# Performance work log

Measured on AMD Instinct MI355X. Metric: run time of the kernel, lower is better.

The kernel has to match this reference:

```python
import jax, jax.numpy as jnp
import numpy as np

S = 256          # seq_len
H = 1024         # hidden_size == input_size (required by inputs + hf add)
NUM_ITER = 1     # interaction module inner iterations
EPS = 1e-5       # BatchNorm1d eps


def setup_inputs() -> dict:
    key = jax.random.key(0)
    ks = jax.random.split(key, 16)
    xav = np.sqrt(2.0 / (H + H))          # xavier_normal for HxH dense
    u = 1.0 / np.sqrt(H)                  # torch LSTMCell default init scale
    inp = {"inputs": jax.random.normal(ks[0], (S, H), jnp.float32)}
    # interaction module dense layers
    for i in range(4):
        inp[f"W{i+1}"] = jax.random.normal(ks[1 + i], (H, H), jnp.float32) * xav
        inp[f"b{i+1}"] = jnp.zeros((H,), jnp.float32)
    # LSTM cells (forward / backward)
    inp["Wih_f"] = jax.random.uniform(ks[5], (4 * H, H), jnp.float32, -u, u)
    inp["Whh_f"] = jax.random.uniform(ks[6], (4 * H, H), jnp.float32, -u, u)
    inp["bih_f"] = jax.random.uniform(ks[7], (4 * H,), jnp.float32, -u, u)
    inp["bhh_f"] = jax.random.uniform(ks[8], (4 * H,), jnp.float32, -u, u)
    inp["Wih_b"] = jax.random.uniform(ks[9], (4 * H, H), jnp.float32, -u, u)
    inp["Whh_b"] = jax.random.uniform(ks[10], (4 * H, H), jnp.float32, -u, u)
    inp["bih_b"] = jax.random.uniform(ks[11], (4 * H,), jnp.float32, -u, u)
    inp["bhh_b"] = jax.random.uniform(ks[12], (4 * H,), jnp.float32, -u, u)
    # BatchNorm1d affine params (default init)
    inp["gamma_f"] = jnp.ones((H,), jnp.float32)
    inp["beta_f"] = jnp.zeros((H,), jnp.float32)
    inp["gamma_b"] = jnp.ones((H,), jnp.float32)
    inp["beta_b"] = jnp.zeros((H,), jnp.float32)
    return inp


def _bn(x, g, b):
    # training-mode BatchNorm1d over the batch (seq) axis, biased variance
    m = jnp.mean(x, axis=0)
    xc = x - m
    v = jnp.mean(xc * xc, axis=0)
    return xc * jax.lax.rsqrt(v + EPS) * g + b


def _lstm_c(x, h, c, Wih, Whh, bih, bhh):
    # torch LSTMCell: returns new cell state only (as used by the module)
    g = x @ Wih.T + bih + h @ Whh.T + bhh
    i, f, gg, o = jnp.split(g, 4)
    return jax.nn.sigmoid(f) * c + jax.nn.sigmoid(i) * jnp.tanh(gg)


def reference(inputs, W1, b1, W2, b2, W3, b3, W4, b4,
              Wih_f, Whh_f, bih_f, bhh_f, Wih_b, Whh_b, bih_b, bhh_b,
              gamma_f, beta_f, gamma_b, beta_b):
    sig = jax.nn.sigmoid

    def interaction(x0, hf, hb):
        for _ in range(NUM_ITER):
            x1 = sig((x0 + hf) @ W1.T + b1)
            hb2 = sig((hb + x1) @ W2.T + b2)
            hf2 = sig((x1 + hf) @ W3.T + b3)
            x0 = sig((hb2 + x1) @ W4.T + b4)
            hf, hb = hf2, hb2
        return x0, hf, hb

    def step(carry, t):
        hf, hb, fc, bc = carry
        _, hf2, hb2 = interaction(inputs, hf, hb)
        out = (hf2 + hb2) * 0.5  # value returned at the last timestep (pre-BN)
        tb = S - 1 - t
        fc = fc.at[t].set(_lstm_c(inputs[t], hf2[t], fc[t], Wih_f, Whh_f, bih_f, bhh_f))
        bc = bc.at[tb].set(_lstm_c(inputs[tb], hb2[tb], bc[tb], Wih_b, Whh_b, bih_b, bhh_b))
        hf_n = _bn(hf2, gamma_f, beta_f)
        hb_n = _bn(hb2, gamma_b, beta_b)
        return (hf_n, hb_n, fc, bc), out

    z = jnp.zeros((S, H), jnp.float32)
    (_, _, _, _), outs = jax.lax.scan(step, (z, z, z, z), jnp.arange(S))
    return outs[-1]  # [S, H]
```

## Files before the change

### kernel.cpp

```cpp
#include <hip/hip_runtime.h>
#include <hip/hip_bf16.h>
#include <math.h>

#define S 256
#define H 1024
#define SH (S*H)
#define EPS 1e-5f

typedef float f32x4 __attribute__((ext_vector_type(4)));
typedef short bf16x8 __attribute__((ext_vector_type(8)));

__device__ __forceinline__ float sigm(float x){ return 1.0f/(1.0f+expf(-x)); }

__device__ __forceinline__ ushort f2bf(float a){
    union { __hip_bfloat16 b; ushort u; } cv;
    cv.b = __float2bfloat16(a);
    return cv.u;
}
__device__ __forceinline__ float bf2f(ushort u){
    union { __hip_bfloat16 b; ushort u; } cv; cv.u = u;
    return __bfloat162float(cv.b);
}

__device__ __forceinline__ int xcd_swizzle(unsigned gbx) {
    return (int)((gbx & 7u) * 32u + (gbx >> 3));
}

__global__ __launch_bounds__(256) void k_pack(const float* __restrict__ W,
                                              ushort* __restrict__ ph,
                                              ushort* __restrict__ pl) {
    int p  = blockIdx.x * 256 + threadIdx.x;
    int l  = p & 63;
    int kt = (p >> 6) & 31;
    int jt = p >> 11;
    int j  = jt * 16 + (l & 15);
    int k0 = kt * 32 + ((l >> 4) << 3);
    const float* src = W + j * H + k0;
    float4 a0 = *(const float4*)src;
    float4 a1 = *(const float4*)(src + 4);
    float av[8] = {a0.x,a0.y,a0.z,a0.w,a1.x,a1.y,a1.z,a1.w};
    bf16x8 vh, vl;
#pragma unroll
    for (int e = 0; e < 8; ++e) {
        ushort h = f2bf(av[e]);
        vh[e] = (short)h;
        vl[e] = (short)f2bf(av[e] - bf2f(h));
    }
    *(bf16x8*)(ph + (size_t)p * 8) = vh;
    *(bf16x8*)(pl + (size_t)p * 8) = vl;
}

__global__ __launch_bounds__(256) void k_init(float* __restrict__ stats,
                                              unsigned* __restrict__ sync) {
    int t = blockIdx.x * 256 + threadIdx.x;
    if (t < 8 * H) stats[t] = 0.0f;
    if (t == 0) { sync[0] = 0u; sync[64] = 0u; }
}

__device__ __forceinline__ void grid_barrier(unsigned* ctrp, unsigned* flagp,
                                             unsigned want) {
    __syncthreads();
    if (threadIdx.x == 0) {
        __threadfence();
        unsigned old = __hip_atomic_fetch_add(ctrp, 1u, __ATOMIC_RELAXED,
                                              __HIP_MEMORY_SCOPE_AGENT);
        if (old == want * 256u - 1u) {
            __hip_atomic_store(flagp, want, __ATOMIC_RELEASE,
                               __HIP_MEMORY_SCOPE_AGENT);
        } else {
            while (__hip_atomic_load(flagp, __ATOMIC_RELAXED,
                                     __HIP_MEMORY_SCOPE_AGENT) < want)
                __builtin_amdgcn_s_sleep(1);
        }
        __threadfence();
    }
    __syncthreads();
}

__global__ __launch_bounds__(256) void k_persist(
    const float* __restrict__ X,
    const ushort* __restrict__ wp1h, const ushort* __restrict__ wp1l,
    const ushort* __restrict__ wp2h, const ushort* __restrict__ wp2l,
    const ushort* __restrict__ wp3h, const ushort* __restrict__ wp3l,
    const float* __restrict__ b1v, const float* __restrict__ b2v,
    const float* __restrict__ b3v,
    const float* __restrict__ gFv, const float* __restrict__ bFv,
    const float* __restrict__ gBv, const float* __restrict__ bBv,
    ushort* __restrict__ A2h, ushort* __restrict__ A2l,
    ushort* __restrict__ A3h, ushort* __restrict__ A3l,
    float* __restrict__ rawf, float* __restrict__ rawb,
    float* __restrict__ stats, float* __restrict__ outp,
    unsigned* __restrict__ syncv)
{
    __shared__ __align__(16) ushort lhs_hi[8192];
    __shared__ __align__(16) ushort lhs_lo[8192];
    __shared__ float scF[H], ofF[H];
    __shared__ float red[4][64][2];

    const int t = threadIdx.x;
    const int g = xcd_swizzle(blockIdx.x);
    const int sb = g & 7, jb = g >> 3;
    const int lane = t & 63, w = t >> 6;
    const int wr = w >> 1, wc = w & 1;
    const int row0 = sb * 32;
    const int jt = jb * 2 + wc;
    const int j = jt * 16 + (lane & 15);
    const int arow = row0 + wr * 16 + (lane & 15);
    const int koff = (lane >> 4) << 3;
    const int srow = row0 + wr * 16 + ((lane >> 4) << 2);
    const float inv = 1.0f / (float)S;

    unsigned* ctrp  = syncv;
    unsigned* flagp = syncv + 64;
    unsigned bgen = 0;

    for (int s = 0; s < S; ++s) {
        const int p = (s + 1) & 1, q = s & 1;
        const int first = (s == 0);
        const float* stP = stats + q * 4 * H;
        float* stA = stats + p * 4 * H;
        const float* rF = rawf + q * SH;
        const float* rB = rawb + q * SH;
        float* wF = rawf + p * SH;
        float* wB = rawb + p * SH;

        if (!first) {
            for (int k = t; k < H; k += 256) {
                float m = stP[k] * inv;
                float v = stP[H + k] * inv - m * m;
                float sc = rsqrtf(v + EPS) * gFv[k];
                scF[k] = sc;
                ofF[k] = bFv[k] - m * sc;
            }
        }
        __syncthreads();

        {
            f32x4 acc0 = {0,0,0,0}, acc1 = {0,0,0,0}, acc2 = {0,0,0,0};
            for (int phase = 0; phase < 4; ++phase) {
                int kbase = phase << 8;
#pragma unroll
                for (int it = 0; it < 4; ++it) {
                    int gg = t + (it << 8);
                    int si = gg & 31, kg = gg >> 5;
                    int k = kbase + (kg << 3);
                    const float* xp = X + (row0 + si) * H + k;
                    float4 x0 = *(const float4*)xp;
                    float4 x1 = *(const float4*)(xp + 4);
                    float a[8] = {x0.x,x0.y,x0.z,x0.w,x1.x,x1.y,x1.z,x1.w};
                    if (!first) {
                        const float* rp = rF + (row0 + si) * H + k;
                        float4 r0 = *(const float4*)rp;
                        float4 r1 = *(const float4*)(rp + 4);
                        float rr[8] = {r0.x,r0.y,r0.z,r0.w,r1.x,r1.y,r1.z,r1.w};
#pragma unroll
                        for (int e = 0; e < 8; ++e)
                            a[e] += rr[e] * scF[k + e] + ofF[k + e];
                    }
                    bf16x8 vh, vl;
#pragma unroll
                    for (int e = 0; e < 8; ++e) {
                        ushort h = f2bf(a[e]);
                        vh[e] = (short)h;
                        vl[e] = (short)f2bf(a[e] - bf2f(h));
                    }
                    int idx = ((((si >> 4) * 8 + (kg >> 2)) * 64) +
                               (((kg & 3) << 4) | (si & 15))) * 8;
                    *(bf16x8*)(lhs_hi + idx) = vh;
                    *(bf16x8*)(lhs_lo + idx) = vl;
                }
                __syncthreads();
                const ushort* bph = wp1h + ((size_t)(jt * 32 + (phase << 3)) * 64 + lane) * 8;
                const ushort* bpl = wp1l + ((size_t)(jt * 32 + (phase << 3)) * 64 + lane) * 8;
                const ushort* ah  = lhs_hi + ((wr * 8) * 64 + lane) * 8;
                const ushort* al  = lhs_lo + ((wr * 8) * 64 + lane) * 8;
#pragma unroll
                for (int kc = 0; kc < 8; ++kc) {
                    bf16x8 a_h = *(const bf16x8*)(ah + kc * 512);
                    bf16x8 a_l = *(const bf16x8*)(al + kc * 512);
                    bf16x8 b_h = *(const bf16x8*)(bph + kc * 512);
                    bf16x8 b_l = *(const bf16x8*)(bpl + kc * 512);
                    acc0 = __builtin_amdgcn_mfma_f32_16x16x32_bf16(a_h, b_h, acc0, 0, 0, 0);
                    acc1 = __builtin_amdgcn_mfma_f32_16x16x32_bf16(a_h, b_l, acc1, 0, 0, 0);
                    acc2 = __builtin_amdgcn_mfma_f32_16x16x32_bf16(a_l, b_h, acc2, 0, 0, 0);
                }
                __syncthreads();
            }

            float bias = b1v[j];
            float scFj = 0.f, ofFj = 0.f, scBj = 0.f, ofBj = 0.f;
            if (!first) {
                scFj = scF[j]; ofFj = ofF[j];
                float m = stP[2 * H + j] * inv;
                float v = stP[3 * H + j] * inv - m * m;
                scBj = rsqrtf(v + EPS) * gBv[j];
                ofBj = bBv[j] - m * scBj;
            }
            f32x4 sum = acc0 + acc1 + acc2;
#pragma unroll
            for (int r = 0; r < 4; ++r) {
                int o = (srow + r) * H + j;
                float x1v = sigm(sum[r] + bias);
                float hb_ = first ? 0.f : rB[o] * scBj + ofBj;
                float hf_ = first ? 0.f : rF[o] * scFj + ofFj;
                float a2 = hb_ + x1v;
                float a3 = x1v + hf_;
                ushort h2 = f2bf(a2);
                A2h[o] = h2;
                A2l[o] = f2bf(a2 - bf2f(h2));
                ushort h3 = f2bf(a3);
                A3h[o] = h3;
                A3l[o] = f2bf(a3 - bf2f(h3));
            }
        }

        grid_barrier(ctrp, flagp, ++bgen);

        if (blockIdx.x == 0) {
            float* z = stats + q * 4 * H;
            for (int k = t; k < 4 * H; k += 256) z[k] = 0.0f;
        }

        float vb[4];
        {
            f32x4 acc0 = {0,0,0,0}, acc1 = {0,0,0,0}, acc2 = {0,0,0,0};
            const ushort* ah = A2h + arow * H + koff;
            const ushort* al = A2l + arow * H + koff;
            const ushort* bh = wp2h + ((size_t)(jt * 32) * 64 + lane) * 8;
            const ushort* bl = wp2l + ((size_t)(jt * 32) * 64 + lane) * 8;
#pragma unroll 8
            for (int kc = 0; kc < 32; ++kc) {
                bf16x8 vah = *(const bf16x8*)(ah + kc * 32);
                bf16x8 val = *(const bf16x8*)(al + kc * 32);
                bf16x8 vbh = *(const bf16x8*)(bh + kc * 512);
                bf16x8 vbl = *(const bf16x8*)(bl + kc * 512);
                acc0 = __builtin_amdgcn_mfma_f32_16x16x32_bf16(vah, vbh, acc0, 0, 0, 0);
                acc1 = __builtin_amdgcn_mfma_f32_16x16x32_bf16(vah, vbl, acc1, 0, 0, 0);
                acc2 = __builtin_amdgcn_mfma_f32_16x16x32_bf16(val, vbh, acc2, 0, 0, 0);
            }
            f32x4 sum = acc0 + acc1 + acc2;
            float bias = b2v[j];
            float ts = 0.f, tq = 0.f;
#pragma unroll
            for (int r = 0; r < 4; ++r) {
                float v = sigm(sum[r] + bias);
                vb[r] = v;
                wB[(srow + r) * H + j] = v;
                ts += v; tq += v * v;
            }
            red[w][lane][0] = ts;
            red[w][lane][1] = tq;
        }
        __syncthreads();
        if (t < 32) {
            int wc2 = t >> 4, jl = t & 15;
            int jj = jb * 32 + wc2 * 16 + jl;
            float ts = 0.f, tq = 0.f;
#pragma unroll
            for (int wr2 = 0; wr2 < 2; ++wr2)
#pragma unroll
                for (int lg = 0; lg < 4; ++lg) {
                    ts += red[wr2 * 2 + wc2][lg * 16 + jl][0];
                    tq += red[wr2 * 2 + wc2][lg * 16 + jl][1];
                }
            atomicAdd(&stA[2 * H + jj], ts);
            atomicAdd(&stA[3 * H + jj], tq);
        }
        __syncthreads();

        {
            f32x4 acc0 = {0,0,0,0}, acc1 = {0,0,0,0}, acc2 = {0,0,0,0};
            const ushort* ah = A3h + arow * H + koff;
            const ushort* al = A3l + arow * H + koff;
            const ushort* bh = wp3h + ((size_t)(jt * 32) * 64 + lane) * 8;
            const ushort* bl = wp3l + ((size_t)(jt * 32) * 64 + lane) * 8;
#pragma unroll 8
            for (int kc = 0; kc < 32; ++kc) {
                bf16x8 vah = *(const bf16x8*)(ah + kc * 32);
                bf16x8 val = *(const bf16x8*)(al + kc * 32);
                bf16x8 vbh = *(const bf16x8*)(bh + kc * 512);
                bf16x8 vbl = *(const bf16x8*)(bl + kc * 512);
                acc0 = __builtin_amdgcn_mfma_f32_16x16x32_bf16(vah, vbh, acc0, 0, 0, 0);
                acc1 = __builtin_amdgcn_mfma_f32_16x16x32_bf16(vah, vbl, acc1, 0, 0, 0);
                acc2 = __builtin_amdgcn_mfma_f32_16x16x32_bf16(val, vbh, acc2, 0, 0, 0);
            }
            f32x4 sum = acc0 + acc1 + acc2;
            float bias = b3v[j];
            float ts = 0.f, tq = 0.f;
#pragma unroll
            for (int r = 0; r < 4; ++r) {
                float v = sigm(sum[r] + bias);
                wF[(srow + r) * H + j] = v;
                if (s == S - 1)
                    outp[(srow + r) * H + j] = 0.5f * (v + vb[r]);
                ts += v; tq += v * v;
            }
            red[w][lane][0] = ts;
            red[w][lane][1] = tq;
        }
        __syncthreads();
        if (t < 32) {
            int wc2 = t >> 4, jl = t & 15;
            int jj = jb * 32 + wc2 * 16 + jl;
            float ts = 0.f, tq = 0.f;
#pragma unroll
            for (int wr2 = 0; wr2 < 2; ++wr2)
#pragma unroll
                for (int lg = 0; lg < 4; ++lg) {
                    ts += red[wr2 * 2 + wc2][lg * 16 + jl][0];
                    tq += red[wr2 * 2 + wc2][lg * 16 + jl][1];
                }
            atomicAdd(&stA[0 * H + jj], ts);
            atomicAdd(&stA[1 * H + jj], tq);
        }

        if (s != S - 1)
            grid_barrier(ctrp, flagp, ++bgen);
    }
}

extern "C" void kernel_launch(void* const* d_in, const int* in_sizes, int n_in,
                              void* d_out, int out_size, void* d_ws, size_t ws_size,
                              hipStream_t stream) {
    (void)in_sizes; (void)n_in; (void)out_size; (void)ws_size;

    const float* X  = (const float*)d_in[0];
    const float* W1 = (const float*)d_in[1];
    const float* b1 = (const float*)d_in[2];
    const float* W2 = (const float*)d_in[3];
    const float* b2 = (const float*)d_in[4];
    const float* W3 = (const float*)d_in[5];
    const float* b3 = (const float*)d_in[6];
    const float* gf = (const float*)d_in[17];
    const float* bf = (const float*)d_in[18];
    const float* gb = (const float*)d_in[19];
    const float* bb = (const float*)d_in[20];

    char* base = (char*)d_ws;
    const size_t MB = 1024 * 1024;
    ushort* wp1h = (ushort*)(base + 0 * MB);
    ushort* wp1l = (ushort*)(base + 2 * MB);
    ushort* wp2h = (ushort*)(base + 4 * MB);
    ushort* wp2l = (ushort*)(base + 6 * MB);
    ushort* wp3h = (ushort*)(base + 8 * MB);
    ushort* wp3l = (ushort*)(base + 10 * MB);
    ushort* A2h  = (ushort*)(base + 12 * MB);
    ushort* A2l  = (ushort*)(base + 12 * MB + 512 * 1024);
    ushort* A3h  = (ushort*)(base + 13 * MB);
    ushort* A3l  = (ushort*)(base + 13 * MB + 512 * 1024);
    float*  rawf = (float*)(base + 14 * MB);
    float*  rawb = (float*)(base + 16 * MB);
    float*  stats= (float*)(base + 18 * MB);
    unsigned* syncv = (unsigned*)(base + 18 * MB + 64 * 1024);

    k_pack<<<512, 256, 0, stream>>>(W1, wp1h, wp1l);
    k_pack<<<512, 256, 0, stream>>>(W2, wp2h, wp2l);
    k_pack<<<512, 256, 0, stream>>>(W3, wp3h, wp3l);
    k_init<<<33, 256, 0, stream>>>(stats, syncv);

    k_persist<<<256, 256, 0, stream>>>(
        X, wp1h, wp1l, wp2h, wp2l, wp3h, wp3l,
        b1, b2, b3, gf, bf, gb, bb,
        A2h, A2l, A3h, A3l,
        rawf, rawb, stats, (float*)d_out, syncv);
}
```

Measured before the change: 16.51 ms.

## Split-K across 8 waves per block and use hierarchical per-XCD grid barrier

```diff
diff --git a/kernel.cpp b/kernel.cpp
--- a/kernel.cpp
+++ b/kernel.cpp
@@ -54,30 +54,32 @@
                                               unsigned* __restrict__ sync) {
     int t = blockIdx.x * 256 + threadIdx.x;
     if (t < 8 * H) stats[t] = 0.0f;
-    if (t == 0) { sync[0] = 0u; sync[64] = 0u; }
-}
-
-__device__ __forceinline__ void grid_barrier(unsigned* ctrp, unsigned* flagp,
-                                             unsigned want) {
+    if (t < 64) sync[t] = 0u;
+}
+
+__device__ __forceinline__ void grid_barrier(unsigned* __restrict__ syncv,
+                                             unsigned want, int xid) {
     __syncthreads();
     if (threadIdx.x == 0) {
         __threadfence();
-        unsigned old = __hip_atomic_fetch_add(ctrp, 1u, __ATOMIC_RELAXED,
+        unsigned old = __hip_atomic_fetch_add(&syncv[xid], 1u, __ATOMIC_RELAXED,
                                               __HIP_MEMORY_SCOPE_AGENT);
-        if (old == want * 256u - 1u) {
-            __hip_atomic_store(flagp, want, __ATOMIC_RELEASE,
-                               __HIP_MEMORY_SCOPE_AGENT);
-        } else {
-            while (__hip_atomic_load(flagp, __ATOMIC_RELAXED,
-                                     __HIP_MEMORY_SCOPE_AGENT) < want)
-                __builtin_amdgcn_s_sleep(1);
-        }
+        if (old == want * 32u - 1u) {
+            unsigned m = __hip_atomic_fetch_add(&syncv[16], 1u, __ATOMIC_RELAXED,
+                                                __HIP_MEMORY_SCOPE_AGENT);
+            if (m == want * 8u - 1u)
+                __hip_atomic_store(&syncv[32], want, __ATOMIC_RELEASE,
+                                   __HIP_MEMORY_SCOPE_AGENT);
+        }
+        while (__hip_atomic_load(&syncv[32], __ATOMIC_RELAXED,
+                                 __HIP_MEMORY_SCOPE_AGENT) < want)
+            __builtin_amdgcn_s_sleep(1);
         __threadfence();
     }
     __syncthreads();
 }
 
-__global__ __launch_bounds__(256) void k_persist(
+__global__ __launch_bounds__(512, 2) void k_persist(
     const float* __restrict__ X,
     const ushort* __restrict__ wp1h, const ushort* __restrict__ wp1l,
     const ushort* __restrict__ wp2h, const ushort* __restrict__ wp2l,
@@ -92,16 +94,21 @@
     float* __restrict__ stats, float* __restrict__ outp,
     unsigned* __restrict__ syncv)
 {
-    __shared__ __align__(16) ushort lhs_hi[8192];
-    __shared__ __align__(16) ushort lhs_lo[8192];
+    __shared__ __align__(16) ushort lhs_hi[32768];
+    __shared__ __align__(16) ushort lhs_lo[32768];
     __shared__ float scF[H], ofF[H];
-    __shared__ float red[4][64][2];
+    __shared__ __align__(16) float redK[8][64][4];
+    __shared__ float redS[4][64][2];
 
     const int t = threadIdx.x;
-    const int g = xcd_swizzle(blockIdx.x);
+    const int bx = blockIdx.x;
+    const int xid = bx & 7;
+    const int g = xcd_swizzle(bx);
     const int sb = g & 7, jb = g >> 3;
     const int lane = t & 63, w = t >> 6;
-    const int wr = w >> 1, wc = w & 1;
+    const int kh = w >> 2;
+    const int ws = w & 3;
+    const int wr = ws >> 1, wc = ws & 1;
     const int row0 = sb * 32;
     const int jt = jb * 2 + wc;
     const int j = jt * 16 + (lane & 15);
@@ -110,8 +117,6 @@
     const int srow = row0 + wr * 16 + ((lane >> 4) << 2);
     const float inv = 1.0f / (float)S;
 
-    unsigned* ctrp  = syncv;
-    unsigned* flagp = syncv + 64;
     unsigned bgen = 0;
 
     for (int s = 0; s < S; ++s) {
@@ -125,7 +130,7 @@
         float* wB = rawb + p * SH;
 
         if (!first) {
-            for (int k = t; k < H; k += 256) {
+            for (int k = t; k < H; k += 512) {
                 float m = stP[k] * inv;
                 float v = stP[H + k] * inv - m * m;
                 float sc = rsqrtf(v + EPS) * gFv[k];
@@ -135,58 +140,63 @@
         }
         __syncthreads();
 
+#pragma unroll
+        for (int it = 0; it < 8; ++it) {
+            int gi = t + (it << 9);
+            int si = gi & 31;
+            int kg = gi >> 5;
+            int k = kg << 3;
+            const float* xp = X + (row0 + si) * H + k;
+            float4 x0 = *(const float4*)xp;
+            float4 x1 = *(const float4*)(xp + 4);
+            float a[8] = {x0.x,x0.y,x0.z,x0.w,x1.x,x1.y,x1.z,x1.w};
+            if (!first) {
+                const float* rp = rF + (row0 + si) * H + k;
+                float4 r0 = *(const float4*)rp;
+                float4 r1 = *(const float4*)(rp + 4);
+                float rr[8] = {r0.x,r0.y,r0.z,r0.w,r1.x,r1.y,r1.z,r1.w};
+#pragma unroll
+                for (int e = 0; e < 8; ++e)
+                    a[e] += rr[e] * scF[k + e] + ofF[k + e];
+            }
+            bf16x8 vh, vl;
+#pragma unroll
+            for (int e = 0; e < 8; ++e) {
+                ushort h = f2bf(a[e]);
+                vh[e] = (short)h;
+                vl[e] = (short)f2bf(a[e] - bf2f(h));
+            }
+            int idx = ((((si >> 4) * 32 + (kg >> 2)) * 64) +
+                       (((kg & 3) << 4) | (si & 15))) * 8;
+            *(bf16x8*)(lhs_hi + idx) = vh;
+            *(bf16x8*)(lhs_lo + idx) = vl;
+        }
+        __syncthreads();
+
         {
             f32x4 acc0 = {0,0,0,0}, acc1 = {0,0,0,0}, acc2 = {0,0,0,0};
-            for (int phase = 0; phase < 4; ++phase) {
-                int kbase = phase << 8;
-#pragma unroll
-                for (int it = 0; it < 4; ++it) {
-                    int gg = t + (it << 8);
-                    int si = gg & 31, kg = gg >> 5;
-                    int k = kbase + (kg << 3);
-                    const float* xp = X + (row0 + si) * H + k;
-                    float4 x0 = *(const float4*)xp;
-                    float4 x1 = *(const float4*)(xp + 4);
-                    float a[8] = {x0.x,x0.y,x0.z,x0.w,x1.x,x1.y,x1.z,x1.w};
-                    if (!first) {
-                        const float* rp = rF + (row0 + si) * H + k;
-                        float4 r0 = *(const float4*)rp;
-                        float4 r1 = *(const float4*)(rp + 4);
-                        float rr[8] = {r0.x,r0.y,r0.z,r0.w,r1.x,r1.y,r1.z,r1.w};
-#pragma unroll
-                        for (int e = 0; e < 8; ++e)
-                            a[e] += rr[e] * scF[k + e] + ofF[k + e];
-                    }
-                    bf16x8 vh, vl;
-#pragma unroll
-                    for (int e = 0; e < 8; ++e) {
-                        ushort h = f2bf(a[e]);
-                        vh[e] = (short)h;
-                        vl[e] = (short)f2bf(a[e] - bf2f(h));
-                    }
-                    int idx = ((((si >> 4) * 8 + (kg >> 2)) * 64) +
-                               (((kg & 3) << 4) | (si & 15))) * 8;
-                    *(bf16x8*)(lhs_hi + idx) = vh;
-                    *(bf16x8*)(lhs_lo + idx) = vl;
-                }
-                __syncthreads();
-                const ushort* bph = wp1h + ((size_t)(jt * 32 + (phase << 3)) * 64 + lane) * 8;
-                const ushort* bpl = wp1l + ((size_t)(jt * 32 + (phase << 3)) * 64 + lane) * 8;
-                const ushort* ah  = lhs_hi + ((wr * 8) * 64 + lane) * 8;
-                const ushort* al  = lhs_lo + ((wr * 8) * 64 + lane) * 8;
-#pragma unroll
-                for (int kc = 0; kc < 8; ++kc) {
-                    bf16x8 a_h = *(const bf16x8*)(ah + kc * 512);
-                    bf16x8 a_l = *(const bf16x8*)(al + kc * 512);
-                    bf16x8 b_h = *(const bf16x8*)(bph + kc * 512);
-                    bf16x8 b_l = *(const bf16x8*)(bpl + kc * 512);
-                    acc0 = __builtin_amdgcn_mfma_f32_16x16x32_bf16(a_h, b_h, acc0, 0, 0, 0);
-                    acc1 = __builtin_amdgcn_mfma_f32_16x16x32_bf16(a_h, b_l, acc1, 0, 0, 0);
-                    acc2 = __builtin_amdgcn_mfma_f32_16x16x32_bf16(a_l, b_h, acc2, 0, 0, 0);
-                }
-                __syncthreads();
-            }
-
+            const int cbase = wr * 32 + kh * 16;
+            const ushort* ah  = lhs_hi + (cbase * 64 + lane) * 8;
+            const ushort* al  = lhs_lo + (cbase * 64 + lane) * 8;
+            const ushort* bph = wp1h + ((size_t)(jt * 32 + kh * 16) * 64 + lane) * 8;
+            const ushort* bpl = wp1l + ((size_t)(jt * 32 + kh * 16) * 64 + lane) * 8;
+#pragma unroll 8
+            for (int kc = 0; kc < 16; ++kc) {
+                bf16x8 a_h = *(const bf16x8*)(ah + kc * 512);
+                bf16x8 a_l = *(const bf16x8*)(al + kc * 512);
+                bf16x8 b_h = *(const bf16x8*)(bph + kc * 512);
+                bf16x8 b_l = *(const bf16x8*)(bpl + kc * 512);
+                acc0 = __builtin_amdgcn_mfma_f32_16x16x32_bf16(a_h, b_h, acc0, 0, 0, 0);
+                acc1 = __builtin_amdgcn_mfma_f32_16x16x32_bf16(a_h, b_l, acc1, 0, 0, 0);
+                acc2 = __builtin_amdgcn_mfma_f32_16x16x32_bf16(a_l, b_h, acc2, 0, 0, 0);
+            }
+            f32x4 part = acc0 + acc1 + acc2;
+            *(f32x4*)&redK[w][lane][0] = part;
+        }
+        __syncthreads();
+
+        if (kh == 0) {
+            f32x4 sum = *(f32x4*)&redK[w][lane][0] + *(f32x4*)&redK[w + 4][lane][0];
             float bias = b1v[j];
             float scFj = 0.f, ofFj = 0.f, scBj = 0.f, ofBj = 0.f;
             if (!first) {
@@ -196,7 +206,6 @@
                 scBj = rsqrtf(v + EPS) * gBv[j];
                 ofBj = bBv[j] - m * scBj;
             }
-            f32x4 sum = acc0 + acc1 + acc2;
 #pragma unroll
             for (int r = 0; r < 4; ++r) {
                 int o = (srow + r) * H + j;
@@ -214,22 +223,23 @@
             }
         }
 
-        grid_barrier(ctrp, flagp, ++bgen);
-
-        if (blockIdx.x == 0) {
+        grid_barrier(syncv, ++bgen, xid);
+
+        if (bx < 8) {
             float* z = stats + q * 4 * H;
-            for (int k = t; k < 4 * H; k += 256) z[k] = 0.0f;
-        }
-
-        float vb[4];
+            z[bx * 512 + t] = 0.0f;
+        }
+
+        float vb[4] = {0,0,0,0};
+
         {
             f32x4 acc0 = {0,0,0,0}, acc1 = {0,0,0,0}, acc2 = {0,0,0,0};
-            const ushort* ah = A2h + arow * H + koff;
-            const ushort* al = A2l + arow * H + koff;
-            const ushort* bh = wp2h + ((size_t)(jt * 32) * 64 + lane) * 8;
-            const ushort* bl = wp2l + ((size_t)(jt * 32) * 64 + lane) * 8;
+            const ushort* ah = A2h + (size_t)arow * H + kh * 512 + koff;
+            const ushort* al = A2l + (size_t)arow * H + kh * 512 + koff;
+            const ushort* bh = wp2h + ((size_t)(jt * 32 + kh * 16) * 64 + lane) * 8;
+            const ushort* bl = wp2l + ((size_t)(jt * 32 + kh * 16) * 64 + lane) * 8;
 #pragma unroll 8
-            for (int kc = 0; kc < 32; ++kc) {
+            for (int kc = 0; kc < 16; ++kc) {
                 bf16x8 vah = *(const bf16x8*)(ah + kc * 32);
                 bf16x8 val = *(const bf16x8*)(al + kc * 32);
                 bf16x8 vbh = *(const bf16x8*)(bh + kc * 512);
@@ -238,7 +248,12 @@
                 acc1 = __builtin_amdgcn_mfma_f32_16x16x32_bf16(vah, vbl, acc1, 0, 0, 0);
                 acc2 = __builtin_amdgcn_mfma_f32_16x16x32_bf16(val, vbh, acc2, 0, 0, 0);
             }
-            f32x4 sum = acc0 + acc1 + acc2;
+            f32x4 part = acc0 + acc1 + acc2;
+            *(f32x4*)&redK[w][lane][0] = part;
+        }
+        __syncthreads();
+        if (kh == 0) {
+            f32x4 sum = *(f32x4*)&redK[w][lane][0] + *(f32x4*)&redK[w + 4][lane][0];
             float bias = b2v[j];
             float ts = 0.f, tq = 0.f;
 #pragma unroll
@@ -248,8 +263,8 @@
                 wB[(srow + r) * H + j] = v;
                 ts += v; tq += v * v;
             }
-            red[w][lane][0] = ts;
-            red[w][lane][1] = tq;
+            redS[ws][lane][0] = ts;
+            redS[ws][lane][1] = tq;
         }
         __syncthreads();
         if (t < 32) {
@@ -260,22 +275,21 @@
             for (int wr2 = 0; wr2 < 2; ++wr2)
 #pragma unroll
                 for (int lg = 0; lg < 4; ++lg) {
-                    ts += red[wr2 * 2 + wc2][lg * 16 + jl][0];
-                    tq += red[wr2 * 2 + wc2][lg * 16 + jl][1];
+                    ts += redS[wr2 * 2 + wc2][lg * 16 + jl][0];
+                    tq += redS[wr2 * 2 + wc2][lg * 16 + jl][1];
                 }
             atomicAdd(&stA[2 * H + jj], ts);
             atomicAdd(&stA[3 * H + jj], tq);
         }
-        __syncthreads();
 
         {
             f32x4 acc0 = {0,0,0,0}, acc1 = {0,0,0,0}, acc2 = {0,0,0,0};
-            const ushort* ah = A3h + arow * H + koff;
-            const ushort* al = A3l + arow * H + koff;
-            const ushort* bh = wp3h + ((size_t)(jt * 32) * 64 + lane) * 8;
-            const ushort* bl = wp3l + ((size_t)(jt * 32) * 64 + lane) * 8;
+            const ushort* ah = A3h + (size_t)arow * H + kh * 512 + koff;
+            const ushort* al = A3l + (size_t)arow * H + kh * 512 + koff;
+            const ushort* bh = wp3h + ((size_t)(jt * 32 + kh * 16) * 64 + lane) * 8;
+            const ushort* bl = wp3l + ((size_t)(jt * 32 + kh * 16) * 64 + lane) * 8;
 #pragma unroll 8
-            for (int kc = 0; kc < 32; ++kc) {
+            for (int kc = 0; kc < 16; ++kc) {
                 bf16x8 vah = *(const bf16x8*)(ah + kc * 32);
                 bf16x8 val = *(const bf16x8*)(al + kc * 32);
                 bf16x8 vbh = *(const bf16x8*)(bh + kc * 512);
@@ -284,7 +298,12 @@
                 acc1 = __builtin_amdgcn_mfma_f32_16x16x32_bf16(vah, vbl, acc1, 0, 0, 0);
                 acc2 = __builtin_amdgcn_mfma_f32_16x16x32_bf16(val, vbh, acc2, 0, 0, 0);
             }
-            f32x4 sum = acc0 + acc1 + acc2;
+            f32x4 part = acc0 + acc1 + acc2;
+            *(f32x4*)&redK[w][lane][0] = part;
+        }
+        __syncthreads();
+        if (kh == 0) {
+            f32x4 sum = *(f32x4*)&redK[w][lane][0] + *(f32x4*)&redK[w + 4][lane][0];
             float bias = b3v[j];
             float ts = 0.f, tq = 0.f;
 #pragma unroll
@@ -295,8 +314,8 @@
                     outp[(srow + r) * H + j] = 0.5f * (v + vb[r]);
                 ts += v; tq += v * v;
             }
-            red[w][lane][0] = ts;
-            red[w][lane][1] = tq;
+            redS[ws][lane][0] = ts;
+            redS[ws][lane][1] = tq;
         }
         __syncthreads();
         if (t < 32) {
@@ -307,15 +326,15 @@
             for (int wr2 = 0; wr2 < 2; ++wr2)
 #pragma unroll
                 for (int lg = 0; lg < 4; ++lg) {
-                    ts += red[wr2 * 2 + wc2][lg * 16 + jl][0];
-                    tq += red[wr2 * 2 + wc2][lg * 16 + jl][1];
+                    ts += redS[wr2 * 2 + wc2][lg * 16 + jl][0];
+                    tq += redS[wr2 * 2 + wc2][lg * 16 + jl][1];
                 }
             atomicAdd(&stA[0 * H + jj], ts);
             atomicAdd(&stA[1 * H + jj], tq);
         }
 
         if (s != S - 1)
-            grid_barrier(ctrp, flagp, ++bgen);
+            grid_barrier(syncv, ++bgen, xid);
     }
 }
 
@@ -358,7 +377,7 @@
     k_pack<<<512, 256, 0, stream>>>(W3, wp3h, wp3l);
     k_init<<<33, 256, 0, stream>>>(stats, syncv);
 
-    k_persist<<<256, 256, 0, stream>>>(
+    k_persist<<<256, 512, 0, stream>>>(
         X, wp1h, wp1l, wp2h, wp2l, wp3h, wp3l,
         b1, b2, b3, gf, bf, gb, bb,
         A2h, A2l, A3h, A3l,
```

Measured after the change: 15.22 ms. 7.8% less time.
